# Performance work log

Hardware: AMD Instinct MI355X
Metric: run time of the kernel (lower is better)

## Reference

```python
import jax, jax.numpy as jnp
import numpy as np

L, D, H, KVH, DH, F, V, SMAX, T = 4, 2048, 16, 8, 128, 6144, 32000, 2048, 1024
EPS = 1e-6
ROPE_THETA = 1e6


def rotate_half(x, axis=-1):
    x1, x2 = jnp.split(x, 2, axis=axis)
    return jnp.concatenate((-x2, x1), axis=axis)


def rms(x, w):
    return w * (x / jnp.sqrt(jnp.mean(x * x, axis=-1, keepdims=True) + EPS))


def setup_inputs() -> dict:
    key = jax.random.key(0)
    ks = jax.random.split(key, 16)
    s = 0.02
    inv_freq = 1.0 / (ROPE_THETA ** (jnp.arange(0, DH, 2, dtype=jnp.float32) / DH))
    ang = jnp.arange(SMAX, dtype=jnp.float32)[:, None] * inv_freq[None, :]  # [SMAX, DH/2]
    cos_emb = jnp.concatenate([jnp.cos(ang), jnp.cos(ang)], axis=-1)  # [SMAX, DH]
    sin_emb = jnp.concatenate([jnp.sin(ang), jnp.sin(ang)], axis=-1)
    sf = DH ** (-0.25)  # scale_factor pre-baked into q_norm/k_norm weights
    return {
        "key_buffer": jnp.zeros((L, KVH, 1, DH, SMAX), jnp.float32),
        "value_buffer": jnp.zeros((L, KVH, 1, SMAX, DH), jnp.float32),
        "input_ids": jax.random.randint(ks[0], (1, T), 0, V, dtype=jnp.int32),
        "attention_mask": jnp.ones((1, T, T), jnp.float32),
        "past_len": 0,
        "embed_data": jax.random.randint(ks[1], (V, D), 0, 256).astype(jnp.uint8),
        "embed_scale": jax.random.uniform(ks[2], (V, 1), jnp.float32, 0.001, 0.02),
        "embed_zero": jax.random.normal(ks[3], (V, 1), jnp.float32) * 0.1,
        "cos_emb": cos_emb,
        "sin_emb": sin_emb,
        "w_in_ln": jnp.ones((L, D), jnp.float32),
        "Wq": jax.random.normal(ks[4], (L, D, H * DH), jnp.float32) * s,
        "Wk": jax.random.normal(ks[5], (L, D, KVH * DH), jnp.float32) * s,
        "Wv": jax.random.normal(ks[6], (L, D, KVH * DH), jnp.float32) * s,
        "w_q_norm": jnp.full((L, DH), sf, jnp.float32),
        "w_k_norm": jnp.full((L, DH), sf, jnp.float32),
        "Wo": jax.random.normal(ks[7], (L, H * DH, D), jnp.float32) * s,
        "w_post_ln": jnp.ones((L, D), jnp.float32),
        "Wgate": jax.random.normal(ks[8], (L, D, F), jnp.float32) * s,
        "Wup": jax.random.normal(ks[9], (L, D, F), jnp.float32) * s,
        "Wdown": jax.random.normal(ks[10], (L, F, D), jnp.float32) * s,
        "w_final_norm": jnp.ones((D,), jnp.float32),
        "W_lm": jax.random.normal(ks[11], (D, V), jnp.float32) * s,
    }


def reference(key_buffer, value_buffer, input_ids, attention_mask, past_len,
              embed_data, embed_scale, embed_zero, cos_emb, sin_emb,
              w_in_ln, Wq, Wk, Wv, w_q_norm, w_k_norm, Wo, w_post_ln,
              Wgate, Wup, Wdown, w_final_norm, W_lm):
    new_len = input_ids.shape[1]
    end = past_len + new_len  # static (past_len is a Python int)
    cos_q = cos_emb[past_len:end]  # [T, DH]
    sin_q = sin_emb[past_len:end]
    # uint8 embedding dequant: e * scale + zero_point
    hidden = embed_data[input_ids].astype(jnp.float32) * embed_scale[input_ids] + embed_zero[input_ids]  # [1,T,D]
    # causal mask: (1 - tril) * -128, sliced to [1, new_len, end], times user mask
    rows = jnp.arange(new_len) + past_len
    cols = jnp.arange(end)
    mask = jnp.where(cols[None, :] <= rows[:, None], 0.0, -128.0)[None] * attention_mask  # [1,T,end]
    G = H // KVH
    for i in range(L):
        hn = rms(hidden, w_in_ln[i])[0]  # [T, D]
        q = (hn @ Wq[i]).reshape(new_len, H, DH)
        q = jnp.transpose(rms(q, w_q_norm[i]), (1, 0, 2))  # [H,T,DH] (sqrt(scale) baked in w_q_norm)
        k = (hn @ Wk[i]).reshape(new_len, KVH, DH)
        k = jnp.transpose(rms(k, w_k_norm[i]), (1, 2, 0))  # [KVH,DH,T]
        v = jnp.transpose((hn @ Wv[i]).reshape(new_len, KVH, DH), (1, 0, 2))  # [KVH,T,DH]
        # RoPE on keys (rotate along DH axis=1)
        k = k * cos_q.T + rotate_half(k, axis=1) * sin_q.T
        key_buffer = jax.lax.dynamic_update_slice(key_buffer, k[None, :, None], (i, 0, 0, 0, past_len))
        value_buffer = jax.lax.dynamic_update_slice(value_buffer, v[None, :, None], (i, 0, 0, past_len, 0))
        # GQA expand: each kv head repeated G times consecutively
        k_exp = jnp.repeat(key_buffer[i, :, 0, :, :end], G, axis=0)  # [H,DH,end]
        v_exp = jnp.repeat(value_buffer[i, :, 0, :end, :], G, axis=0)  # [H,end,DH]
        q_rot = q * cos_q[None] + rotate_half(q, axis=-1) * sin_q[None]
        scores = jnp.einsum('htd,hds->hts', q_rot, k_exp) + mask
        attn = jax.nn.softmax(scores, axis=-1)
        ctx = jnp.transpose(jnp.einsum('hts,hsd->htd', attn, v_exp), (1, 0, 2)).reshape(1, new_len, H * DH)
        hidden = hidden + ctx @ Wo[i]
        hn2 = rms(hidden, w_post_ln[i])
        hidden = hidden + (jax.nn.silu(hn2 @ Wgate[i]) * (hn2 @ Wup[i])) @ Wdown[i]
    last = rms(hidden[:, -1], w_final_norm)  # [1, D]
    logits = last @ W_lm  # [1, V]
    tok_id = jnp.argmax(logits, axis=-1, keepdims=True).astype(jnp.int32)
    new_seq_len = jnp.array([end], dtype=jnp.int32)
    return (tok_id, key_buffer, value_buffer, new_seq_len)
```

## Files before the change

### kernel.cpp

```cpp
#include <hip/hip_runtime.h>
#include <cstdint>

#define L_ 4
#define D_ 2048
#define H_ 16
#define KVH_ 8
#define DH_ 128
#define F_ 6144
#define V_ 32000
#define SMAX_ 2048
#define T_ 1024
#define EPS_ 1e-6f
#define QB 32
#define SB 128
#define ZQK 4194304
#define ZS2 2097152

typedef unsigned short u16;
typedef unsigned int u32;
typedef float fvec4 __attribute__((ext_vector_type(4)));
typedef float f32x4 __attribute__((ext_vector_type(4)));
typedef __bf16 bf16x8 __attribute__((ext_vector_type(8)));

__device__ __forceinline__ u16 f2bf(float f) {
  union { float f; u32 u; } a; a.f = f;
  u32 u = a.u;
  return (u16)((u + 0x7FFFu + ((u >> 16) & 1u)) >> 16);
}
__device__ __forceinline__ float bf2f(u16 h) {
  union { u32 u; float f; } a; a.u = (u32)h << 16; return a.f;
}
__device__ __forceinline__ fvec4 bf4(uint2 u) {
  union { u32 i; float f; } a, b, c, d;
  a.i = u.x << 16; b.i = u.x & 0xFFFF0000u;
  c.i = u.y << 16; d.i = u.y & 0xFFFF0000u;
  fvec4 r; r[0] = a.f; r[1] = b.f; r[2] = c.f; r[3] = d.f; return r;
}

__device__ __forceinline__ void gld16(const void* g, void* l) {
  __builtin_amdgcn_global_load_lds(
      (const __attribute__((address_space(1))) void*)g,
      (__attribute__((address_space(3))) void*)l, 16, 0, 0);
}

__global__ void embed_k(const int* __restrict__ ids, const void* __restrict__ edata,
                        const float* __restrict__ esc, const float* __restrict__ ez,
                        float* __restrict__ hidden)
{
  const int* ei = (const int*)edata;
  int chk = ei[threadIdx.x & 63];
  bool ok = ((unsigned)chk) <= 255u;
  bool is_i32 = (__ballot(ok) == ~0ULL);
  int t = blockIdx.x;
  int id = ids[t];
  float sc = esc[id], zp = ez[id];
  size_t base = (size_t)id * D_;
  const uint8_t* eb = (const uint8_t*)edata;
  for (int d = threadIdx.x; d < D_; d += 256) {
    float e = is_i32 ? (float)ei[base + d] : (float)eb[base + d];
    hidden[(size_t)t * D_ + d] = e * sc + zp;
  }
}

__device__ __forceinline__ void convT_body(const float* __restrict__ W, int N,
                                           int nb, int kb, int K, int rb,
                                           u16* __restrict__ WT, int gu, float* tile)
{
  int n0 = nb * 64, k0 = kb * 64;
  int tid = threadIdx.x;
  int lk = tid >> 4, n4 = (tid & 15) * 4;
#pragma unroll
  for (int i = 0; i < 4; ++i) {
    int kr = i * 16 + lk;
    fvec4 v = *(const fvec4*)(W + (size_t)(k0 + kr) * N + n0 + n4);
#pragma unroll
    for (int j = 0; j < 4; ++j) tile[(n4 + j) * 65 + kr] = v[j];
  }
  __syncthreads();
  int n = tid >> 2, kq = (tid & 3) * 16;
  int f = n0 + n;
  int row = gu ? (rb + ((f >> 4) << 5) + (f & 15)) : (rb + f);
  union { u16 h[16]; uint4 q[2]; } o;
#pragma unroll
  for (int i = 0; i < 16; ++i) o.h[i] = f2bf(tile[n * 65 + kq + i]);
  u16* op = WT + (size_t)row * K + k0 + kq;
  *(uint4*)op = o.q[0];
  *(uint4*)(op + 8) = o.q[1];
}

template<int NZ>
__device__ __forceinline__ void rms_body(int idx, float* __restrict__ x,
                                         const u16* __restrict__ p, int zs,
                                         const float* __restrict__ w,
                                         u16* __restrict__ out)
{
  int t = idx * 4 + (threadIdx.x >> 6);
  int l = threadIdx.x & 63;
  fvec4* xr = (fvec4*)(x + (size_t)t * D_);
  fvec4 v[8];
#pragma unroll
  for (int j = 0; j < 8; ++j) v[j] = xr[l + 64 * j];
  if (NZ > 0) {
#pragma unroll
    for (int z = 0; z < NZ; ++z) {
      const uint2* a = (const uint2*)(p + (size_t)z * zs + (size_t)t * D_);
#pragma unroll
      for (int j = 0; j < 8; ++j) v[j] += bf4(a[l + 64 * j]);
    }
#pragma unroll
    for (int j = 0; j < 8; ++j) xr[l + 64 * j] = v[j];
  }
  float s = 0.f;
#pragma unroll
  for (int j = 0; j < 8; ++j)
    s += v[j][0]*v[j][0] + v[j][1]*v[j][1] + v[j][2]*v[j][2] + v[j][3]*v[j][3];
#pragma unroll
  for (int m = 32; m; m >>= 1) s += __shfl_xor(s, m);
  float inv = rsqrtf(s * (1.f / D_) + EPS_);
  const fvec4* wr = (const fvec4*)w;
  u16* orow = out + (size_t)t * D_;
#pragma unroll
  for (int j = 0; j < 8; ++j) {
    fvec4 wv = wr[l + 64 * j];
    uint2 o;
    o.x = (u32)f2bf(wv[0]*v[j][0]*inv) | ((u32)f2bf(wv[1]*v[j][1]*inv) << 16);
    o.y = (u32)f2bf(wv[2]*v[j][2]*inv) | ((u32)f2bf(wv[3]*v[j][3]*inv) << 16);
    *(uint2*)(orow + (l + 64 * j) * 4) = o;
  }
}

template<int NZ>
__global__ __launch_bounds__(256)
void convqkv_rms_k(const float* __restrict__ Wq, const float* __restrict__ Wk,
                   const float* __restrict__ Wv, u16* __restrict__ WT,
                   float* __restrict__ x, const u16* __restrict__ p,
                   const float* __restrict__ w, u16* __restrict__ out)
{
  __shared__ float tile[64 * 65];
  int bx = blockIdx.x, y = blockIdx.y;
  if (bx < 64) {
    const float* W; int N, nb, rb;
    if (bx < 32)      { W = Wq; N = 2048; nb = bx;      rb = 0; }
    else if (bx < 48) { W = Wk; N = 1024; nb = bx - 32; rb = 2048; }
    else              { W = Wv; N = 1024; nb = bx - 48; rb = 3072; }
    convT_body(W, N, nb, y, 2048, rb, WT, 0, tile);
  } else {
    rms_body<NZ>((bx - 64) * 32 + y, x, p, ZS2, w, out);
  }
}

__global__ __launch_bounds__(256)
void rms_k(float* __restrict__ x, const u16* __restrict__ p,
           const float* __restrict__ w, u16* __restrict__ out)
{
  rms_body<4>(blockIdx.x, x, p, ZS2, w, out);
}

template<int EPI>
__device__ __forceinline__ void gemm_body(const u16* __restrict__ A,
                                          const u16* __restrict__ B,
                                          u16* __restrict__ Cb,
                                          int K, int Ks, int ldC, long long zStride,
                                          int bx, int by, int bz, char* smem)
{
  u16* lA = (u16*)smem;
  u16* lB = (u16*)(smem + 16384);
  const u16* Ab = A + (size_t)by * 128 * K;
  const u16* Bb = B + (size_t)bx * 128 * K;
  int kz = bz * Ks;

  int tid = threadIdx.x;
  int l = tid & 63;
  int wid = tid >> 6;
  int wr = wid >> 1, wc = wid & 1;
  int lrow = l & 15, lk = l >> 4;

  f32x4 acc[4][4] = {};

  for (int k0 = 0; k0 < Ks; k0 += 64) {
#pragma unroll
    for (int r = 0; r < 4; ++r) {
      int c = r * 256 + tid;
      int row = c >> 3, g = c & 7;
      int kel = kz + k0 + ((g ^ (row & 7)) << 3);
      gld16(Ab + (size_t)row * K + kel, (char*)lA + c * 16);
      gld16(Bb + (size_t)row * K + kel, (char*)lB + c * 16);
    }
    __syncthreads();
#pragma unroll
    for (int kk = 0; kk < 2; ++kk) {
      bf16x8 av[4], bv[4];
      int kbyte = (kk * 32 + lk * 8) * 2;
#pragma unroll
      for (int m = 0; m < 4; ++m) {
        int row = wr * 64 + m * 16 + lrow;
        int byt = (row * 128 + kbyte) ^ ((row & 7) << 4);
        av[m] = *(const bf16x8*)((const char*)lA + byt);
      }
#pragma unroll
      for (int n = 0; n < 4; ++n) {
        int row = wc * 64 + n * 16 + lrow;
        int byt = (row * 128 + kbyte) ^ ((row & 7) << 4);
        bv[n] = *(const bf16x8*)((const char*)lB + byt);
      }
#pragma unroll
      for (int m = 0; m < 4; ++m)
#pragma unroll
        for (int n = 0; n < 4; ++n)
          acc[m][n] = __builtin_amdgcn_mfma_f32_16x16x32_bf16(av[m], bv[n], acc[m][n], 0, 0, 0);
    }
    __syncthreads();
  }

  int grow0 = by * 128 + wr * 64 + lk * 4;
  if (EPI == 3) {
    int fcol0 = bx * 64 + wc * 32 + lrow;
#pragma unroll
    for (int m = 0; m < 4; ++m)
#pragma unroll
      for (int np = 0; np < 2; ++np)
#pragma unroll
        for (int r = 0; r < 4; ++r) {
          float g = acc[m][2 * np][r], u = acc[m][2 * np + 1][r];
          float val = g / (1.f + __expf(-g)) * u;
          Cb[(size_t)(grow0 + m * 16 + r) * ldC + fcol0 + np * 16] = f2bf(val);
        }
    return;
  }
  u16* Cz = Cb + (long long)bz * zStride;
  int gcol0 = bx * 128 + wc * 64 + lrow;
#pragma unroll
  for (int m = 0; m < 4; ++m)
#pragma unroll
    for (int n = 0; n < 4; ++n)
#pragma unroll
      for (int r = 0; r < 4; ++r)
        Cz[(size_t)(grow0 + m * 16 + r) * ldC + gcol0 + n * 16] = f2bf(acc[m][n][r]);
}

template<int EPI>
__global__ __launch_bounds__(256)
void gemm_bt(const u16* __restrict__ A, const u16* __restrict__ B,
             u16* __restrict__ Cb, int K, int Ks, int ldC, long long zStride)
{
  __shared__ char smem[32768];
  gemm_body<EPI>(A, B, Cb, K, Ks, ldC, zStride, blockIdx.x, blockIdx.y, blockIdx.z, smem);
}

__global__ __launch_bounds__(256)
void qkvgemm_conv_k(const u16* __restrict__ hn, const u16* __restrict__ wTqkv,
                    u16* __restrict__ P,
                    const float* __restrict__ Wo, u16* __restrict__ wTo,
                    const float* __restrict__ Wg, const float* __restrict__ Wu,
                    u16* __restrict__ wTgu,
                    const float* __restrict__ Wd, u16* __restrict__ wTwd)
{
  __shared__ char smem[32768];
  int bx = blockIdx.x;
  if (bx < 512) {
    gemm_body<0>(hn, wTqkv, P, 2048, 1024, 4096, ZQK,
                 bx & 31, (bx >> 5) & 7, bx >> 8, smem);
  } else if (bx < 1536) {
    int cb = bx - 512;
    convT_body(Wo, 2048, cb & 31, cb >> 5, 2048, 0, wTo, 0, (float*)smem);
  } else if (bx < 7680) {
    int cb = bx - 1536;
    int x = cb % 192, y = cb / 192;
    const float* W = x < 96 ? Wg : Wu;
    convT_body(W, 6144, x < 96 ? x : x - 96, y, 2048, x < 96 ? 0 : 16, wTgu, 1, (float*)smem);
  } else {
    int cb = bx - 7680;
    int xp = cb % 96, y = cb / 96;
    convT_body(Wd, 2048, xp & 31, ((xp >> 5) << 5) + y, 6144, 0, wTwd, 0, (float*)smem);
  }
}

__global__ __launch_bounds__(256)
void qkvpost_k(const u16* __restrict__ p0, const u16* __restrict__ p1,
               const float* __restrict__ wq, const float* __restrict__ wk,
               const float* __restrict__ cosT, const float* __restrict__ sinT,
               const int* __restrict__ plp,
               u16* __restrict__ qr, u16* __restrict__ kr, u16* __restrict__ vT,
               float* __restrict__ key_out, float* __restrict__ val_out)
{
  __shared__ float tile[64][132];
  int t0 = blockIdx.x * 64;
  int z = blockIdx.y;
  int pl = plp[0];
  int tid = threadIdx.x;
  int cb = z < 16 ? z * 128 : (z < 24 ? 2048 + (z - 16) * 128 : 3072 + (z - 24) * 128);

  {
    int r = tid >> 5;
    int c = (tid & 31) * 4;
#pragma unroll
    for (int i = 0; i < 8; ++i) {
      int row = i * 8 + r;
      size_t off = (size_t)(t0 + row) * 4096 + cb + c;
      fvec4 v = bf4(*(const uint2*)(p0 + off)) + bf4(*(const uint2*)(p1 + off));
      *(fvec4*)&tile[row][c] = v;
    }
  }
  __syncthreads();

  if (z < 24) {
    int row = tid >> 2, q = tid & 3;
    int dbase = q * 32, pbase = (q ^ 2) * 32;
    const float* wn = z < 16 ? wq : wk;
    float sgn = (q < 2) ? -1.f : 1.f;
    fvec4 xv[8];
    float ss = 0.f;
#pragma unroll
    for (int j = 0; j < 8; ++j) {
      xv[j] = *(const fvec4*)&tile[row][dbase + j * 4];
      ss += xv[j][0]*xv[j][0] + xv[j][1]*xv[j][1] + xv[j][2]*xv[j][2] + xv[j][3]*xv[j][3];
    }
    ss += __shfl_xor(ss, 1);
    ss += __shfl_xor(ss, 2);
    float inv = rsqrtf(ss * (1.f / 128.f) + EPS_);
    int p = pl + t0 + row;
    float rv[32];
#pragma unroll
    for (int j = 0; j < 8; ++j) {
      fvec4 xo = *(const fvec4*)&tile[row][pbase + j * 4];
      fvec4 wv = *(const fvec4*)(wn + dbase + j * 4);
      fvec4 wo = *(const fvec4*)(wn + pbase + j * 4);
      fvec4 cs = *(const fvec4*)(cosT + (size_t)p * 128 + dbase + j * 4);
      fvec4 sn = *(const fvec4*)(sinT + (size_t)p * 128 + dbase + j * 4);
#pragma unroll
      for (int e = 0; e < 4; ++e) {
        float xn = wv[e] * xv[j][e] * inv;
        float xp = wo[e] * xo[e] * inv;
        rv[j * 4 + e] = xn * cs[e] + sgn * xp * sn[e];
      }
    }
    union { u32 w[8]; uint4 q4[2]; } ob;
    u16* orow = (z < 16 ? qr + ((size_t)z * T_ + t0 + row) * 128
                        : kr + ((size_t)(z - 16) * T_ + t0 + row) * 128) + dbase;
#pragma unroll
    for (int j = 0; j < 8; ++j)
      ob.w[j] = (u32)f2bf(rv[2 * j]) | ((u32)f2bf(rv[2 * j + 1]) << 16);
    *(uint4*)orow = ob.q4[0];
    *(uint4*)(orow + 8) = ob.q4[1];
#pragma unroll
    for (int j = 0; j < 8; ++j)
      ob.w[j] = (u32)f2bf(rv[16 + 2 * j]) | ((u32)f2bf(rv[17 + 2 * j]) << 16);
    *(uint4*)(orow + 16) = ob.q4[0];
    *(uint4*)(orow + 24) = ob.q4[1];

    if (z >= 16) {
      __syncthreads();
#pragma unroll
      for (int j = 0; j < 8; ++j) {
        fvec4 v; v[0] = rv[j*4]; v[1] = rv[j*4+1]; v[2] = rv[j*4+2]; v[3] = rv[j*4+3];
        *(fvec4*)&tile[row][dbase + j * 4] = v;
      }
      __syncthreads();
      int d = tid >> 1, cc = (tid & 1) * 32;
      float* kp = key_out + ((size_t)(z - 16) * 128 + d) * SMAX_ + pl + t0 + cc;
      if ((pl & 3) == 0) {
#pragma unroll
        for (int j4 = 0; j4 < 8; ++j4) {
          fvec4 v;
#pragma unroll
          for (int e = 0; e < 4; ++e) v[e] = tile[cc + j4 * 4 + e][d];
          *(fvec4*)(kp + j4 * 4) = v;
        }
      } else {
        for (int j = 0; j < 32; ++j) kp[j] = tile[cc + j][d];
      }
    }
  } else {
    int kv = z - 24;
    int row = tid >> 2, q = tid & 3;
    float* vp = val_out + ((size_t)kv * SMAX_ + pl + t0 + row) * 128 + q * 32;
#pragma unroll
    for (int j = 0; j < 8; ++j)
      *(fvec4*)(vp + j * 4) = *(const fvec4*)&tile[row][q * 32 + j * 4];
    int d = tid >> 1, cc = (tid & 1) * 32;
    union { u32 w[16]; uint4 q4[4]; } ob;
    u16* tp = vT + ((size_t)kv * 128 + d) * T_ + t0 + cc;
#pragma unroll
    for (int j = 0; j < 16; ++j)
      ob.w[j] = (u32)f2bf(tile[cc + 2 * j][d]) | ((u32)f2bf(tile[cc + 2 * j + 1][d]) << 16);
    *(uint4*)tp = ob.q4[0];
    *(uint4*)(tp + 8) = ob.q4[1];
    *(uint4*)(tp + 16) = ob.q4[2];
    *(uint4*)(tp + 24) = ob.q4[3];
  }
}

__global__ __launch_bounds__(256)
void flash_k(const u16* __restrict__ qr, const u16* __restrict__ kr,
             const u16* __restrict__ vTb, const float* __restrict__ am,
             const int* __restrict__ plp, u16* __restrict__ ctx)
{
  __shared__ u16 lQ[QB * DH_];
  __shared__ u16 lKV[SB * DH_];
  __shared__ u16 lP[QB * SB];
  __shared__ float lMax[2][2][16];
  __shared__ float lSum[2][2][16];
  __shared__ float lScale[QB];
  __shared__ float lFin[QB];

  int qt = gridDim.x - 1 - blockIdx.x;
  int h = blockIdx.y;
  int kvh = h >> 1;
  int pl = plp[0];
  int tid = threadIdx.x;
  int l = tid & 63, w = tid >> 6;
  int lrow = l & 15, lk = l >> 4;
  int tb = w & 1, sh = w >> 1;
  int tcol = tb * 16 + lrow;

  const u16* Qb = qr + ((size_t)h * T_ + qt * QB) * DH_;
  const u16* Kb = kr + (size_t)kvh * T_ * DH_;
  const u16* Vb = vTb + (size_t)kvh * DH_ * T_;

#pragma unroll
  for (int r = 0; r < 2; ++r) {
    int c = r * 256 + tid;
    int row = c >> 4, g = c & 15;
    gld16(Qb + (size_t)row * DH_ + ((g ^ (row & 7)) << 3), (char*)lQ + c * 16);
  }

  float m_run = -3.0e38f, l_run = 0.f;
  f32x4 acc_o[2][2] = {};

  int t_lo = qt * QB;
  int s_hi = min(T_, t_lo + QB + pl);
  int nt = (s_hi + SB - 1) / SB;
  int tg = t_lo + tcol;

  for (int it = 0; it < nt; ++it) {
    int s0 = it * SB;
#pragma unroll
    for (int r = 0; r < 8; ++r) {
      int c = r * 256 + tid;
      int row = c >> 4, g = c & 15;
      gld16(Kb + (size_t)(s0 + row) * DH_ + ((g ^ (row & 7)) << 3), (char*)lKV + c * 16);
    }
    __syncthreads();

    f32x4 acc_s[4] = {};
#pragma unroll
    for (int kk = 0; kk < 4; ++kk) {
      int kbyte = kk * 64 + lk * 16;
      int trow = tb * 16 + lrow;
      bf16x8 bq = *(const bf16x8*)((const char*)lQ + ((trow * 256 + kbyte) ^ ((trow & 7) << 4)));
#pragma unroll
      for (int m = 0; m < 4; ++m) {
        int srow = sh * 64 + m * 16 + lrow;
        bf16x8 ak = *(const bf16x8*)((const char*)lKV + ((srow * 256 + kbyte) ^ ((srow & 7) << 4)));
        acc_s[m] = __builtin_amdgcn_mfma_f32_16x16x32_bf16(ak, bq, acc_s[m], 0, 0, 0);
      }
    }
    __syncthreads();

#pragma unroll
    for (int r = 0; r < 8; ++r) {
      int c = r * 256 + tid;
      int row = c >> 4, g = c & 15;
      gld16(Vb + (size_t)row * T_ + s0 + ((g ^ (row & 7)) << 3), (char*)lKV + c * 16);
    }

    bool full = (s0 + SB <= t_lo + pl + 1);
    float sv[4][4];
    float vmax = -3.0e38f;
    if (full) {
#pragma unroll
      for (int m = 0; m < 4; ++m)
#pragma unroll
        for (int r = 0; r < 4; ++r) {
          float val = acc_s[m][r]; sv[m][r] = val; vmax = fmaxf(vmax, val);
        }
    } else {
#pragma unroll
      for (int m = 0; m < 4; ++m) {
        int sg = s0 + sh * 64 + m * 16 + lk * 4;
        fvec4 a4 = *(const fvec4*)(am + (size_t)tg * T_ + sg);
#pragma unroll
        for (int r = 0; r < 4; ++r) {
          float val = acc_s[m][r] + ((sg + r <= tg + pl) ? 0.f : -128.f * a4[r]);
          sv[m][r] = val; vmax = fmaxf(vmax, val);
        }
      }
    }
    vmax = fmaxf(vmax, __shfl_xor(vmax, 16));
    vmax = fmaxf(vmax, __shfl_xor(vmax, 32));
    if (lk == 0) lMax[tb][sh][lrow] = vmax;
    __syncthreads();

    float om = fmaxf(lMax[tb][0][lrow], lMax[tb][1][lrow]);
    float m_new = fmaxf(m_run, om);
    float corr = __expf(m_run - m_new);
    float psum = 0.f;
    u32 pw[4][2];
#pragma unroll
    for (int m = 0; m < 4; ++m) {
      float p0 = __expf(sv[m][0] - m_new);
      float p1 = __expf(sv[m][1] - m_new);
      float p2 = __expf(sv[m][2] - m_new);
      float p3 = __expf(sv[m][3] - m_new);
      psum += (p0 + p1) + (p2 + p3);
      pw[m][0] = (u32)f2bf(p0) | ((u32)f2bf(p1) << 16);
      pw[m][1] = (u32)f2bf(p2) | ((u32)f2bf(p3) << 16);
    }
    psum += __shfl_xor(psum, 16);
    psum += __shfl_xor(psum, 32);
    if (lk == 0) lSum[tb][sh][lrow] = psum;
    if (lk == 0 && sh == 0) lScale[tcol] = corr;
#pragma unroll
    for (int m = 0; m < 4; ++m) {
      int byt = (tcol * 256 + sh * 128 + m * 32 + lk * 8) ^ ((tcol & 7) << 4);
      *(uint2*)((char*)lP + byt) = make_uint2(pw[m][0], pw[m][1]);
    }
    __syncthreads();

    l_run = l_run * corr + lSum[tb][0][lrow] + lSum[tb][1][lrow];
    m_run = m_new;
#pragma unroll
    for (int m = 0; m < 2; ++m) {
      fvec4 c4 = *(const fvec4*)&lScale[m * 16 + lk * 4];
#pragma unroll
      for (int n = 0; n < 2; ++n)
#pragma unroll
        for (int r = 0; r < 4; ++r) acc_o[m][n][r] *= c4[r];
    }
#pragma unroll
    for (int kk = 0; kk < 4; ++kk) {
      int kbyte = kk * 64 + lk * 16;
      bf16x8 ap[2], bv[2];
#pragma unroll
      for (int m = 0; m < 2; ++m) {
        int trow = m * 16 + lrow;
        ap[m] = *(const bf16x8*)((const char*)lP + ((trow * 256 + kbyte) ^ ((trow & 7) << 4)));
      }
#pragma unroll
      for (int n = 0; n < 2; ++n) {
        int drow = w * 32 + n * 16 + lrow;
        bv[n] = *(const bf16x8*)((const char*)lKV + ((drow * 256 + kbyte) ^ ((drow & 7) << 4)));
      }
#pragma unroll
      for (int m = 0; m < 2; ++m)
#pragma unroll
        for (int n = 0; n < 2; ++n)
          acc_o[m][n] = __builtin_amdgcn_mfma_f32_16x16x32_bf16(ap[m], bv[n], acc_o[m][n], 0, 0, 0);
    }
    __syncthreads();
  }

  if (lk == 0 && sh == 0) lFin[tcol] = l_run;
  __syncthreads();
#pragma unroll
  for (int m = 0; m < 2; ++m) {
    fvec4 s4 = *(const fvec4*)&lFin[m * 16 + lk * 4];
#pragma unroll
    for (int r = 0; r < 4; ++r) {
      float inv = 1.f / s4[r];
      int trow = t_lo + m * 16 + lk * 4 + r;
      u16* crow = ctx + (size_t)trow * (H_ * DH_) + h * DH_;
#pragma unroll
      for (int n = 0; n < 2; ++n) {
        int d = w * 32 + n * 16 + lrow;
        crow[d] = f2bf(acc_o[m][n][r] * inv);
      }
    }
  }
}

__global__ void lmgemv_k(const float* __restrict__ x, const u16* __restrict__ p,
                         const float* __restrict__ wfin, const float* __restrict__ Wlm,
                         float* __restrict__ part)
{
  __shared__ float ls[256];
  __shared__ float sm[4];
  int tid = threadIdx.x;
  int c = blockIdx.y;
  float xv[8];
  float s = 0.f;
#pragma unroll
  for (int j = 0; j < 8; ++j) {
    int d = j * 256 + tid;
    float v = x[d] + bf2f(p[d]) + bf2f(p[ZS2 + d]) + bf2f(p[2 * ZS2 + d]) + bf2f(p[3 * ZS2 + d]);
    xv[j] = v; s += v * v;
  }
#pragma unroll
  for (int m = 32; m; m >>= 1) s += __shfl_xor(s, m);
  if ((tid & 63) == 0) sm[tid >> 6] = s;
  __syncthreads();
  s = sm[0] + sm[1] + sm[2] + sm[3];
  float inv = rsqrtf(s * (1.f / D_) + EPS_);
#pragma unroll
  for (int j = 0; j < 8; ++j)
    if (j == c) ls[tid] = wfin[j * 256 + tid] * xv[j] * inv;
  __syncthreads();
  int v = blockIdx.x * 256 + tid;
  const float* Wp = Wlm + (size_t)c * 256 * V_ + v;
  float acc = 0.f;
#pragma unroll 8
  for (int d = 0; d < 256; d++) acc += ls[d] * Wp[(size_t)d * V_];
  part[(size_t)c * V_ + v] = acc;
}

__global__ void amax_part_k(const float* __restrict__ part, float2* __restrict__ out)
{
  __shared__ float sv[4];
  __shared__ int si[4];
  int v = blockIdx.x * 256 + threadIdx.x;
  float val = 0.f;
#pragma unroll
  for (int c = 0; c < 8; c++) val += part[(size_t)c * V_ + v];
  float bv = val; int bi = v;
#pragma unroll
  for (int m = 32; m; m >>= 1) {
    float ov = __shfl_xor(bv, m);
    int oi = __shfl_xor(bi, m);
    if (ov > bv || (ov == bv && oi < bi)) { bv = ov; bi = oi; }
  }
  if ((threadIdx.x & 63) == 0) { sv[threadIdx.x >> 6] = bv; si[threadIdx.x >> 6] = bi; }
  __syncthreads();
  if (threadIdx.x == 0) {
    for (int w = 1; w < 4; w++)
      if (sv[w] > bv || (sv[w] == bv && si[w] < bi)) { bv = sv[w]; bi = si[w]; }
    out[blockIdx.x] = make_float2(bv, (float)bi);
  }
}

__global__ void finalize_k(const float2* __restrict__ part, int np,
                           const int* __restrict__ plp, float* __restrict__ dout,
                           unsigned long long lastoff)
{
  if (threadIdx.x == 0) {
    float bv = part[0].x; int bi = (int)part[0].y;
    for (int b = 1; b < np; b++) {
      float v = part[b].x; int i = (int)part[b].y;
      if (v > bv || (v == bv && i < bi)) { bv = v; bi = i; }
    }
    dout[0] = (float)bi;
    dout[lastoff] = (float)(plp[0] + T_);
  }
}

extern "C" void kernel_launch(void* const* d_in, const int* in_sizes, int n_in,
                              void* d_out, int out_size, void* d_ws, size_t ws_size,
                              hipStream_t stream)
{
  (void)in_sizes; (void)n_in; (void)out_size; (void)ws_size;

  const float* key_in  = (const float*)d_in[0];
  const float* val_in  = (const float*)d_in[1];
  const int*   ids     = (const int*)d_in[2];
  const float* am      = (const float*)d_in[3];
  const int*   plp     = (const int*)d_in[4];
  const void*  edata   = d_in[5];
  const float* esc     = (const float*)d_in[6];
  const float* ez      = (const float*)d_in[7];
  const float* cosT    = (const float*)d_in[8];
  const float* sinT    = (const float*)d_in[9];
  const float* w_in_ln = (const float*)d_in[10];
  const float* Wq      = (const float*)d_in[11];
  const float* Wk      = (const float*)d_in[12];
  const float* Wv      = (const float*)d_in[13];
  const float* wqn     = (const float*)d_in[14];
  const float* wkn     = (const float*)d_in[15];
  const float* Wo      = (const float*)d_in[16];
  const float* wpost   = (const float*)d_in[17];
  const float* Wg      = (const float*)d_in[18];
  const float* Wu      = (const float*)d_in[19];
  const float* Wd      = (const float*)d_in[20];
  const float* wfin    = (const float*)d_in[21];
  const float* Wlm     = (const float*)d_in[22];

  float* out = (float*)d_out;
  const size_t KVN = (size_t)L_ * KVH_ * DH_ * SMAX_;
  float* key_out = out + 1;
  float* val_out = out + 1 + KVN;
  unsigned long long lastoff = 1 + 2 * KVN;

  char* ws = (char*)d_ws;
  u16*   wTqkv  = (u16*)  (ws + 0);
  u16*   mlp    = (u16*)  (ws + 0);
  float* lpart  = (float*)(ws + 16777216);
  float2* amaxp = (float2*)(ws + 17825792);
  u16*   wTo    = (u16*)  (ws + 33554432);
  u16*   wTgu   = (u16*)  (ws + 41943040);
  u16*   wTwd   = (u16*)  (ws + 92274688);
  u16*   P      = (u16*)  (ws + 117440512);
  u16*   hn     = (u16*)  (ws + 134217728);
  u16*   qr     = (u16*)  (ws + 138412032);
  u16*   kr     = (u16*)  (ws + 142606336);
  u16*   vT     = (u16*)  (ws + 144703488);
  u16*   ctx    = (u16*)  (ws + 146800640);
  float* hidden = (float*)(ws + 150994944);

  hipMemcpyAsync(key_out, key_in, KVN * sizeof(float), hipMemcpyDeviceToDevice, stream);
  hipMemcpyAsync(val_out, val_in, KVN * sizeof(float), hipMemcpyDeviceToDevice, stream);
  embed_k<<<T_, 256, 0, stream>>>(ids, edata, esc, ez, hidden);

  for (int i = 0; i < L_; i++) {
    if (i == 0)
      convqkv_rms_k<0><<<dim3(72, 32), 256, 0, stream>>>(
          Wq, Wk, Wv, wTqkv, hidden, nullptr, w_in_ln, hn);
    else
      convqkv_rms_k<4><<<dim3(72, 32), 256, 0, stream>>>(
          Wq + (size_t)i * 4194304, Wk + (size_t)i * 2097152, Wv + (size_t)i * 2097152,
          wTqkv, hidden, P, w_in_ln + (size_t)i * D_, hn);

    qkvgemm_conv_k<<<10752, 256, 0, stream>>>(
        hn, wTqkv, P,
        Wo + (size_t)i * 4194304, wTo,
        Wg + (size_t)i * 12582912, Wu + (size_t)i * 12582912, wTgu,
        Wd + (size_t)i * 12582912, wTwd);

    qkvpost_k<<<dim3(16, 32), 256, 0, stream>>>(P, P + ZQK,
        wqn + (size_t)i * DH_, wkn + (size_t)i * DH_, cosT, sinT, plp,
        qr, kr, vT,
        key_out + (size_t)i * KVH_ * DH_ * SMAX_,
        val_out + (size_t)i * KVH_ * SMAX_ * DH_);

    flash_k<<<dim3(T_ / QB, H_), 256, 0, stream>>>(qr, kr, vT, am, plp, ctx);

    gemm_bt<0><<<dim3(16, 8, 4), 256, 0, stream>>>(ctx, wTo, P, 2048, 512, 2048, ZS2);

    rms_k<<<256, 256, 0, stream>>>(hidden, P, wpost + (size_t)i * D_, hn);

    gemm_bt<3><<<dim3(96, 8, 1), 256, 0, stream>>>(hn, wTgu, mlp, 2048, 2048, 6144, 0);

    gemm_bt<0><<<dim3(16, 8, 4), 256, 0, stream>>>(mlp, wTwd, P, 6144, 1536, 2048, ZS2);
  }

  lmgemv_k<<<dim3(V_ / 256, 8), 256, 0, stream>>>(
      hidden + (size_t)(T_ - 1) * D_, P + (size_t)(T_ - 1) * D_, wfin, Wlm, lpart);
  amax_part_k<<<V_ / 256, 256, 0, stream>>>(lpart, amaxp);
  finalize_k<<<1, 64, 0, stream>>>(amaxp, V_ / 256, plp, out, lastoff);
}
```

Baseline: 1.073 ms.

## Spread weight fp32->bf16 transposes across GEMM kernels to overlap conversion with compute

Weight transpose/conversion work, previously piled into one big kernel after the QKV GEMM, is now split up. Each conversion rides along with an earlier kernel: Wo with the RMS kernel, Wgate/Wup with the QKV GEMM, Wdown with the gate/up GEMM, and the next layer's QKV weights with the down-projection GEMM. The first layer's QKV conversion is fused with the embedding into a prologue kernel. The aim is to balance memory-bound conversion against compute-bound GEMMs and fill idle CUs, at the cost of moving the mlp buffer to a new workspace offset to avoid aliasing with wTqkv.

```diff
diff --git a/kernel.cpp b/kernel.cpp
--- a/kernel.cpp
+++ b/kernel.cpp
@@ -43,15 +43,16 @@
       (__attribute__((address_space(3))) void*)l, 16, 0, 0);
 }
 
-__global__ void embed_k(const int* __restrict__ ids, const void* __restrict__ edata,
-                        const float* __restrict__ esc, const float* __restrict__ ez,
-                        float* __restrict__ hidden)
+__device__ __forceinline__ void embed_body(int t, const int* __restrict__ ids,
+                                           const void* __restrict__ edata,
+                                           const float* __restrict__ esc,
+                                           const float* __restrict__ ez,
+                                           float* __restrict__ hidden)
 {
   const int* ei = (const int*)edata;
   int chk = ei[threadIdx.x & 63];
   bool ok = ((unsigned)chk) <= 255u;
   bool is_i32 = (__ballot(ok) == ~0ULL);
-  int t = blockIdx.x;
   int id = ids[t];
   float sc = esc[id], zp = ez[id];
   size_t base = (size_t)id * D_;
@@ -88,6 +89,36 @@
   *(uint4*)(op + 8) = o.q[1];
 }
 
+__device__ __forceinline__ void convqkv_route(int x, int y,
+                                              const float* __restrict__ Wq,
+                                              const float* __restrict__ Wk,
+                                              const float* __restrict__ Wv,
+                                              u16* __restrict__ WT, float* tile)
+{
+  const float* W; int N, nb, rb;
+  if (x < 32)      { W = Wq; N = 2048; nb = x;      rb = 0; }
+  else if (x < 48) { W = Wk; N = 1024; nb = x - 32; rb = 2048; }
+  else             { W = Wv; N = 1024; nb = x - 48; rb = 3072; }
+  convT_body(W, N, nb, y, 2048, rb, WT, 0, tile);
+}
+
+__global__ __launch_bounds__(256)
+void prologue_k(const int* __restrict__ ids, const void* __restrict__ edata,
+                const float* __restrict__ esc, const float* __restrict__ ez,
+                float* __restrict__ hidden,
+                const float* __restrict__ Wq, const float* __restrict__ Wk,
+                const float* __restrict__ Wv, u16* __restrict__ WT)
+{
+  __shared__ float tile[64 * 65];
+  int bx = blockIdx.x;
+  if (bx < 1024) {
+    embed_body(bx, ids, edata, esc, ez, hidden);
+  } else {
+    int cb = bx - 1024;
+    convqkv_route(cb >> 5, cb & 31, Wq, Wk, Wv, WT, tile);
+  }
+}
+
 template<int NZ>
 __device__ __forceinline__ void rms_body(int idx, float* __restrict__ x,
                                          const u16* __restrict__ p, int zs,
@@ -131,21 +162,16 @@
 
 template<int NZ>
 __global__ __launch_bounds__(256)
-void convqkv_rms_k(const float* __restrict__ Wq, const float* __restrict__ Wk,
-                   const float* __restrict__ Wv, u16* __restrict__ WT,
-                   float* __restrict__ x, const u16* __restrict__ p,
-                   const float* __restrict__ w, u16* __restrict__ out)
+void rms_convwo_k(float* __restrict__ x, const u16* __restrict__ p,
+                  const float* __restrict__ w, u16* __restrict__ out,
+                  const float* __restrict__ Wo, u16* __restrict__ wTo)
 {
   __shared__ float tile[64 * 65];
   int bx = blockIdx.x, y = blockIdx.y;
-  if (bx < 64) {
-    const float* W; int N, nb, rb;
-    if (bx < 32)      { W = Wq; N = 2048; nb = bx;      rb = 0; }
-    else if (bx < 48) { W = Wk; N = 1024; nb = bx - 32; rb = 2048; }
-    else              { W = Wv; N = 1024; nb = bx - 48; rb = 3072; }
-    convT_body(W, N, nb, y, 2048, rb, WT, 0, tile);
+  if (bx < 32) {
+    convT_body(Wo, 2048, bx, y, 2048, 0, wTo, 0, tile);
   } else {
-    rms_body<NZ>((bx - 64) * 32 + y, x, p, ZS2, w, out);
+    rms_body<NZ>((bx - 32) * 32 + y, x, p, ZS2, w, out);
   }
 }
 
@@ -248,30 +274,55 @@
 }
 
 __global__ __launch_bounds__(256)
-void qkvgemm_conv_k(const u16* __restrict__ hn, const u16* __restrict__ wTqkv,
-                    u16* __restrict__ P,
-                    const float* __restrict__ Wo, u16* __restrict__ wTo,
-                    const float* __restrict__ Wg, const float* __restrict__ Wu,
-                    u16* __restrict__ wTgu,
-                    const float* __restrict__ Wd, u16* __restrict__ wTwd)
+void qkvgemm_convgu_k(const u16* __restrict__ hn, const u16* __restrict__ wTqkv,
+                      u16* __restrict__ P,
+                      const float* __restrict__ Wg, const float* __restrict__ Wu,
+                      u16* __restrict__ wTgu)
 {
   __shared__ char smem[32768];
   int bx = blockIdx.x;
   if (bx < 512) {
     gemm_body<0>(hn, wTqkv, P, 2048, 1024, 4096, ZQK,
                  bx & 31, (bx >> 5) & 7, bx >> 8, smem);
-  } else if (bx < 1536) {
+  } else {
     int cb = bx - 512;
-    convT_body(Wo, 2048, cb & 31, cb >> 5, 2048, 0, wTo, 0, (float*)smem);
-  } else if (bx < 7680) {
-    int cb = bx - 1536;
     int x = cb % 192, y = cb / 192;
     const float* W = x < 96 ? Wg : Wu;
     convT_body(W, 6144, x < 96 ? x : x - 96, y, 2048, x < 96 ? 0 : 16, wTgu, 1, (float*)smem);
+  }
+}
+
+__global__ __launch_bounds__(256)
+void gugemm_convwd_k(const u16* __restrict__ hn, const u16* __restrict__ wTgu,
+                     u16* __restrict__ mlp,
+                     const float* __restrict__ Wd, u16* __restrict__ wTwd)
+{
+  __shared__ char smem[32768];
+  int bx = blockIdx.x;
+  if (bx < 768) {
+    gemm_body<3>(hn, wTgu, mlp, 2048, 2048, 6144, 0, bx % 96, bx / 96, 0, smem);
   } else {
-    int cb = bx - 7680;
+    int cb = bx - 768;
     int xp = cb % 96, y = cb / 96;
     convT_body(Wd, 2048, xp & 31, ((xp >> 5) << 5) + y, 6144, 0, wTwd, 0, (float*)smem);
+  }
+}
+
+template<int CONV>
+__global__ __launch_bounds__(256)
+void wdgemm_convqkv_k(const u16* __restrict__ mlp, const u16* __restrict__ wTwd,
+                      u16* __restrict__ P,
+                      const float* __restrict__ Wq, const float* __restrict__ Wk,
+                      const float* __restrict__ Wv, u16* __restrict__ wTqkv)
+{
+  __shared__ char smem[32768];
+  int bx = blockIdx.x;
+  if (bx < 512) {
+    gemm_body<0>(mlp, wTwd, P, 6144, 1536, 2048, ZS2,
+                 bx & 15, (bx >> 4) & 7, bx >> 7, smem);
+  } else if (CONV) {
+    int cb = bx - 512;
+    convqkv_route(cb >> 5, cb & 31, Wq, Wk, Wv, wTqkv, (float*)smem);
   }
 }
 
@@ -680,7 +731,6 @@
 
   char* ws = (char*)d_ws;
   u16*   wTqkv  = (u16*)  (ws + 0);
-  u16*   mlp    = (u16*)  (ws + 0);
   float* lpart  = (float*)(ws + 16777216);
   float2* amaxp = (float2*)(ws + 17825792);
   u16*   wTo    = (u16*)  (ws + 33554432);
@@ -692,26 +742,24 @@
   u16*   kr     = (u16*)  (ws + 142606336);
   u16*   vT     = (u16*)  (ws + 144703488);
   u16*   ctx    = (u16*)  (ws + 146800640);
+  u16*   mlp    = (u16*)  (ws + 138412032);
   float* hidden = (float*)(ws + 150994944);
 
   hipMemcpyAsync(key_out, key_in, KVN * sizeof(float), hipMemcpyDeviceToDevice, stream);
   hipMemcpyAsync(val_out, val_in, KVN * sizeof(float), hipMemcpyDeviceToDevice, stream);
-  embed_k<<<T_, 256, 0, stream>>>(ids, edata, esc, ez, hidden);
+
+  prologue_k<<<3072, 256, 0, stream>>>(ids, edata, esc, ez, hidden, Wq, Wk, Wv, wTqkv);
 
   for (int i = 0; i < L_; i++) {
     if (i == 0)
-      convqkv_rms_k<0><<<dim3(72, 32), 256, 0, stream>>>(
-          Wq, Wk, Wv, wTqkv, hidden, nullptr, w_in_ln, hn);
+      rms_convwo_k<0><<<dim3(40, 32), 256, 0, stream>>>(
+          hidden, nullptr, w_in_ln, hn, Wo, wTo);
     else
-      convqkv_rms_k<4><<<dim3(72, 32), 256, 0, stream>>>(
-          Wq + (size_t)i * 4194304, Wk + (size_t)i * 2097152, Wv + (size_t)i * 2097152,
-          wTqkv, hidden, P, w_in_ln + (size_t)i * D_, hn);
-
-    qkvgemm_conv_k<<<10752, 256, 0, stream>>>(
-        hn, wTqkv, P,
-        Wo + (size_t)i * 4194304, wTo,
-        Wg + (size_t)i * 12582912, Wu + (size_t)i * 12582912, wTgu,
-        Wd + (size_t)i * 12582912, wTwd);
+      rms_convwo_k<4><<<dim3(40, 32), 256, 0, stream>>>(
+          hidden, P, w_in_ln + (size_t)i * D_, hn, Wo + (size_t)i * 4194304, wTo);
+
+    qkvgemm_convgu_k<<<6656, 256, 0, stream>>>(
+        hn, wTqkv, P, Wg + (size_t)i * 12582912, Wu + (size_t)i * 12582912, wTgu);
 
     qkvpost_k<<<dim3(16, 32), 256, 0, stream>>>(P, P + ZQK,
         wqn + (size_t)i * DH_, wkn + (size_t)i * DH_, cosT, sinT, plp,
@@ -725,9 +773,17 @@
 
     rms_k<<<256, 256, 0, stream>>>(hidden, P, wpost + (size_t)i * D_, hn);
 
-    gemm_bt<3><<<dim3(96, 8, 1), 256, 0, stream>>>(hn, wTgu, mlp, 2048, 2048, 6144, 0);
-
-    gemm_bt<0><<<dim3(16, 8, 4), 256, 0, stream>>>(mlp, wTwd, P, 6144, 1536, 2048, ZS2);
+    gugemm_convwd_k<<<3840, 256, 0, stream>>>(
+        hn, wTgu, mlp, Wd + (size_t)i * 12582912, wTwd);
+
+    if (i < L_ - 1)
+      wdgemm_convqkv_k<1><<<2560, 256, 0, stream>>>(
+          mlp, wTwd, P,
+          Wq + (size_t)(i + 1) * 4194304, Wk + (size_t)(i + 1) * 2097152,
+          Wv + (size_t)(i + 1) * 2097152, wTqkv);
+    else
+      wdgemm_convqkv_k<0><<<512, 256, 0, stream>>>(
+          mlp, wTwd, P, nullptr, nullptr, nullptr, nullptr);
   }
 
   lmgemv_k<<<dim3(V_ / 256, 8), 256, 0, stream>>>(
```

New measurement: 1.088 ms. Within noise of the previous version (+1.4%).
